# Performance work log

Measured on AMD Instinct MI355X. Metric: run time of the kernel, lower is better.

## Reference

```python
import jax, jax.numpy as jnp
import numpy as np
import math

D_MODEL = 2048
N_HEADS = 16
BATCH = 2
SEQ = 2048
ALIBI_BIAS_MAX = 8


def alibi_bias(n_heads, seq_len, alibi_bias_max=8):
    # matches torch alibi_bias(full=False): shape [1, n_heads, 1, seq_len]
    dist = jnp.arange(1 - seq_len, 1, dtype=jnp.float32).reshape(1, 1, 1, seq_len)
    m = jnp.arange(1, n_heads + 1, dtype=jnp.float32) * (alibi_bias_max / n_heads)
    slopes = 1.0 / (2.0 ** m).reshape(1, n_heads, 1, 1)
    return dist * slopes


def setup_inputs() -> dict:
    key = jax.random.key(0)
    ks = jax.random.split(key, 5)
    d = D_MODEL
    scale = 1.0 / math.sqrt(d)
    x = jax.random.normal(ks[0], (BATCH, SEQ, d), dtype=jnp.float32)
    w_qkv = jax.random.normal(ks[1], (3 * d, d), dtype=jnp.float32) * scale
    b_qkv = jnp.zeros((3 * d,), dtype=jnp.float32)
    w_out = jax.random.normal(ks[2], (d, d), dtype=jnp.float32) * scale
    b_out = jnp.zeros((d,), dtype=jnp.float32)
    attn_mask = alibi_bias(N_HEADS, SEQ, ALIBI_BIAS_MAX)
    return {"x": x, "attn_mask": attn_mask, "w_qkv": w_qkv, "b_qkv": b_qkv,
            "w_out": w_out, "b_out": b_out}


def reference(x, attn_mask, w_qkv, b_qkv, w_out, b_out):
    B, S, D = x.shape
    H = N_HEADS
    hd = D // H
    # packed QKV projection
    qkv = x @ w_qkv.T + b_qkv                      # [B,S,3D]
    qkv = qkv.reshape(B, S, 3, H, hd)
    q, k, v = qkv[:, :, 0], qkv[:, :, 1], qkv[:, :, 2]  # [B,S,H,hd]
    scores = jnp.einsum('bqhd,bkhd->bhqk', q, k) * (1.0 / math.sqrt(hd))
    scores = scores + attn_mask                    # ALiBi additive bias [1,H,1,S]
    causal = jnp.tril(jnp.ones((S, S), dtype=bool))
    scores = jnp.where(causal, scores, -jnp.inf)
    probs = jax.nn.softmax(scores, axis=-1)        # [B,H,S,S]
    ctx = jnp.einsum('bhqk,bkhd->bqhd', probs, v).reshape(B, S, D)
    return ctx @ w_out.T + b_out
```

## Files before the change

### kernel.cpp

```cpp
#include <hip/hip_runtime.h>
#include <math.h>

typedef unsigned short u16;
typedef __attribute__((ext_vector_type(8))) short short8;
typedef __attribute__((ext_vector_type(4))) float f32x4;

#define MFMA16x16x32(a, b, c) __builtin_amdgcn_mfma_f32_16x16x32_bf16((a), (b), (c), 0, 0, 0)
#define GLL16(g, s)                                                        \
  __builtin_amdgcn_global_load_lds(                                        \
      (const __attribute__((address_space(1))) void*)(g),                  \
      (__attribute__((address_space(3))) void*)(s), 16, 0, 0)

__device__ __forceinline__ u16 f32_to_bf16(float x) {
  union { float f; unsigned u; } v; v.f = x;
  unsigned r = v.u + 0x7FFFu + ((v.u >> 16) & 1u);
  return (u16)(r >> 16);
}

__device__ __forceinline__ void cvt4(const float* in, u16* out, int j) {
  float4 v = ((const float4*)in)[j];
  ushort4 o;
  o.x = f32_to_bf16(v.x);
  o.y = f32_to_bf16(v.y);
  o.z = f32_to_bf16(v.z);
  o.w = f32_to_bf16(v.w);
  ((ushort4*)out)[j] = o;
}

__global__ void cvt_all(const float* __restrict__ x, const float* __restrict__ wq,
                        const float* __restrict__ wo, u16* __restrict__ xb,
                        u16* __restrict__ wqb, u16* __restrict__ wob) {
  const int stride = gridDim.x * blockDim.x;
  const int i = blockIdx.x * blockDim.x + threadIdx.x;
  for (int j = i; j < 2097152; j += stride) cvt4(x, xb, j);
  for (int j = i; j < 3145728; j += stride) cvt4(wq, wqb, j);
  for (int j = i; j < 1048576; j += stride) cvt4(wo, wob, j);
}

template <int OUT_BF16>
__global__ __launch_bounds__(256, 3) void gemm_k32(
    const u16* __restrict__ A,
    const u16* __restrict__ B,
    const float* __restrict__ bias,
    void* __restrict__ C,
    int M, int N, int K)
{
  __shared__ u16 As[3][4096];
  __shared__ u16 Bs[3][4096];

  const int tid = threadIdx.x;
  const int w = tid >> 6, l = tid & 63;
  const int l15 = l & 15, l4 = l >> 4;
  const int wm = w >> 1, wn = w & 1;
  const long bm = (long)blockIdx.y * 128, bn = (long)blockIdx.x * 128;
  const int NT = K >> 5;

  const int h = (l & 7) ^ (l >> 3);
  const int rowoff = 2 * (l >> 3) + (h >> 2);
  const int colofs = (h & 3) * 8;
  const int c0 = (w & 1) * 4;
  const u16* sbase = (w < 2) ? (A + bm * (long)K) : (B + bn * (long)K);
  const u16* src0 = sbase + (long)(16 * (c0 + 0) + rowoff) * K + colofs;
  const u16* src1 = sbase + (long)(16 * (c0 + 1) + rowoff) * K + colofs;
  const u16* src2 = sbase + (long)(16 * (c0 + 2) + rowoff) * K + colofs;
  const u16* src3 = sbase + (long)(16 * (c0 + 3) + rowoff) * K + colofs;

#define STAGE4(tt)                                                            \
  do {                                                                        \
    const int _b = (tt) % 3;                                                  \
    const long _ko = (long)(tt) * 32;                                         \
    u16* _d = (w < 2) ? &As[_b][c0 * 512] : &Bs[_b][c0 * 512];                \
    GLL16(src0 + _ko, _d);                                                    \
    GLL16(src1 + _ko, _d + 512);                                              \
    GLL16(src2 + _ko, _d + 1024);                                             \
    GLL16(src3 + _ko, _d + 1536);                                             \
  } while (0)

  const f32x4 z4 = {0.f, 0.f, 0.f, 0.f};
  f32x4 acc[4][4];
  #pragma unroll
  for (int m = 0; m < 4; ++m)
    #pragma unroll
    for (int n = 0; n < 4; ++n) acc[m][n] = z4;

  const int inner = ((l15 & 1) * 64 + l4 * 16) ^ ((l15 >> 1) << 4);
  const int rbase = (l15 >> 1) * 128 + inner;
  const int aOfs = wm * 4096 + rbase;
  const int bOfs = wn * 4096 + rbase;

  STAGE4(0);
  STAGE4(1);
  asm volatile("s_waitcnt vmcnt(4)" ::: "memory");
  __builtin_amdgcn_s_barrier();

  for (int t = 0; t < NT; ++t) {
    const char* aT = (const char*)&As[t % 3][0];
    const char* bT = (const char*)&Bs[t % 3][0];
    short8 af[4], bf[4];
    #pragma unroll
    for (int m = 0; m < 4; ++m) af[m] = *(const short8*)(aT + aOfs + m * 1024);
    #pragma unroll
    for (int n = 0; n < 4; ++n) bf[n] = *(const short8*)(bT + bOfs + n * 1024);
    if (t + 2 < NT) {
      STAGE4(t + 2);
      asm volatile("s_waitcnt vmcnt(4) lgkmcnt(0)" ::: "memory");
    } else {
      asm volatile("s_waitcnt vmcnt(0) lgkmcnt(0)" ::: "memory");
    }
    __builtin_amdgcn_s_setprio(1);
    #pragma unroll
    for (int m = 0; m < 4; ++m)
      #pragma unroll
      for (int n = 0; n < 4; ++n)
        acc[m][n] = MFMA16x16x32(af[m], bf[n], acc[m][n]);
    __builtin_amdgcn_s_setprio(0);
    __builtin_amdgcn_s_barrier();
  }
#undef STAGE4

  #pragma unroll
  for (int m = 0; m < 4; ++m) {
    const long row0 = bm + wm * 64 + m * 16 + l4 * 4;
    #pragma unroll
    for (int n = 0; n < 4; ++n) {
      const long col = bn + wn * 64 + n * 16 + l15;
      const float bv = bias[col];
      #pragma unroll
      for (int r = 0; r < 4; ++r) {
        const float v = acc[m][n][r] + bv;
        if (OUT_BF16)
          ((u16*)C)[(row0 + r) * (long)N + col] = f32_to_bf16(v);
        else
          ((float*)C)[(row0 + r) * (long)N + col] = v;
      }
    }
  }
}

__global__ __launch_bounds__(256) void repack_kv(
    const u16* __restrict__ qkv, u16* __restrict__ kimg, u16* __restrict__ vimg)
{
  const int t = blockIdx.x;
  const int h = blockIdx.y, b = blockIdx.z;
  const int tid = threadIdx.x;
  __shared__ u16 Vl[64][136];

  const long qbase = ((long)(b * 2048 + t * 64)) * 6144 + h * 128;
  u16* kout = kimg + (((long)(b * 16 + h) * 32 + t) * 8192);
  u16* vout = vimg + (((long)(b * 16 + h) * 32 + t) * 8192);

  #pragma unroll
  for (int i = 0; i < 4; ++i) {
    const int j = tid + i * 256;
    {
      const int r = j >> 4, c8 = (j & 15) * 8;
      uint4 v = *(const uint4*)(qkv + qbase + (long)r * 6144 + 4096 + c8);
      *(uint4*)(&Vl[r][c8]) = v;
    }
    {
      const int byte = j * 16;
      const int r = byte >> 8;
      const int wv = (byte & 255) ^ ((r & 7) << 4);
      const int d0 = wv >> 1;
      uint4 v = *(const uint4*)(qkv + qbase + (long)r * 6144 + 2048 + d0);
      *(uint4*)(kout + j * 8) = v;
    }
  }
  __syncthreads();
  #pragma unroll
  for (int i = 0; i < 4; ++i) {
    const int j = tid + i * 256;
    const int byte = j * 16;
    const int d = byte >> 7;
    const int wv = (byte & 127) ^ ((d & 7) << 4);
    const int k0 = wv >> 1;
    u16 tmp[8];
    #pragma unroll
    for (int m = 0; m < 8; ++m) tmp[m] = Vl[k0 + m][d];
    *(uint4*)(vout + j * 8) = *(const uint4*)tmp;
  }
}

__global__ __launch_bounds__(256) void attn_kernel(
    const u16* __restrict__ qkv,
    const u16* __restrict__ kimg,
    const u16* __restrict__ vimg,
    u16* __restrict__ ctx)
{
  const int S = 2048, NHD = 6144, NT = 32;
  const int p = blockIdx.x, h = blockIdx.y, b = blockIdx.z;
  const int tid = threadIdx.x;
  const int w = tid >> 6, l = tid & 63;
  const int l15 = l & 15, l4 = l >> 4;

  __shared__ u16 Ks[64 * 128];
  __shared__ u16 Vt[128 * 64];
  __shared__ u16 Ps[4][16 * 64];

  const float LOG2E = 1.44269504088896f;
  const float c1 = 0.08838834764831845f * LOG2E;
  const float slope2 = exp2f(-0.5f * (float)(h + 1)) * LOG2E;

  const f32x4 z4 = {0.f, 0.f, 0.f, 0.f};

  for (int pass = 0; pass < 2; ++pass) {
    const int qblk = pass ? (NT - 1 - p) : p;
    const int qb0 = qblk * 64;

    short8 qf[4];
    {
      const int qrow = qb0 + w * 16 + l15;
      const u16* qp = qkv + (long)(b * S + qrow) * NHD + h * 128 + l4 * 8;
      #pragma unroll
      for (int kc = 0; kc < 4; ++kc) qf[kc] = *(const short8*)(qp + kc * 32);
    }

    f32x4 o[8];
    #pragma unroll
    for (int i = 0; i < 8; ++i) o[i] = z4;
    float m_r[4] = {-3.0e38f, -3.0e38f, -3.0e38f, -3.0e38f};
    float l_r[4] = {0.f, 0.f, 0.f, 0.f};

    for (int kt = 0; kt <= qblk; ++kt) {
      const u16* ksrc = kimg + (((long)(b * 16 + h) * NT + kt) * 8192);
      const u16* vsrc = vimg + (((long)(b * 16 + h) * NT + kt) * 8192);
      #pragma unroll
      for (int i = 0; i < 4; ++i) {
        const int chunk = w * 4 + i;
        __builtin_amdgcn_global_load_lds(
            (const __attribute__((address_space(1))) void*)(ksrc + chunk * 512 + l * 8),
            (__attribute__((address_space(3))) void*)(Ks + chunk * 512), 16, 0, 0);
        __builtin_amdgcn_global_load_lds(
            (const __attribute__((address_space(1))) void*)(vsrc + chunk * 512 + l * 8),
            (__attribute__((address_space(3))) void*)(Vt + chunk * 512), 16, 0, 0);
      }
      __syncthreads();

      f32x4 sf[4];
      #pragma unroll
      for (int nt = 0; nt < 4; ++nt) sf[nt] = z4;
      #pragma unroll
      for (int nt = 0; nt < 4; ++nt) {
        const int krow = nt * 16 + l15;
        #pragma unroll
        for (int kc = 0; kc < 4; ++kc) {
          int kbyte = (krow * 256 + kc * 64 + l4 * 16) ^ ((krow & 7) << 4);
          const short8 kf = *(const short8*)((const char*)Ks + kbyte);
          sf[nt] = MFMA16x16x32(qf[kc], kf, sf[nt]);
        }
      }

      float add_nt[4];
      int kg_nt[4];
      #pragma unroll
      for (int nt = 0; nt < 4; ++nt) {
        kg_nt[nt] = kt * 64 + nt * 16 + l15;
        add_nt[nt] = slope2 * (float)(kg_nt[nt] - (S - 1));
      }
      const bool diag = (kt == qblk);
      float sc[4][4], mxv[4];
      #pragma unroll
      for (int r = 0; r < 4; ++r) {
        const int qg = qb0 + w * 16 + l4 * 4 + r;
        #pragma unroll
        for (int nt = 0; nt < 4; ++nt) {
          float s = sf[nt][r] * c1 + add_nt[nt];
          if (diag && kg_nt[nt] > qg) s = -3.0e38f;
          sc[r][nt] = s;
        }
        mxv[r] = fmaxf(fmaxf(sc[r][0], sc[r][1]), fmaxf(sc[r][2], sc[r][3]));
      }
      #pragma unroll
      for (int d = 1; d < 16; d <<= 1) {
        #pragma unroll
        for (int r = 0; r < 4; ++r)
          mxv[r] = fmaxf(mxv[r], __shfl_xor(mxv[r], d, 64));
      }
      float alpha[4], sum[4];
      #pragma unroll
      for (int r = 0; r < 4; ++r) {
        const float mnew = fmaxf(m_r[r], mxv[r]);
        sum[r] = 0.f;
        #pragma unroll
        for (int nt = 0; nt < 4; ++nt) {
          const float pv = exp2f(sc[r][nt] - mnew);
          sc[r][nt] = pv;
          sum[r] += pv;
        }
        alpha[r] = exp2f(m_r[r] - mnew);
        m_r[r] = mnew;
      }
      #pragma unroll
      for (int d = 1; d < 16; d <<= 1) {
        #pragma unroll
        for (int r = 0; r < 4; ++r) sum[r] += __shfl_xor(sum[r], d, 64);
      }
      #pragma unroll
      for (int r = 0; r < 4; ++r) l_r[r] = l_r[r] * alpha[r] + sum[r];

      #pragma unroll
      for (int r = 0; r < 4; ++r) {
        const int qrow_l = l4 * 4 + r;
        #pragma unroll
        for (int nt = 0; nt < 4; ++nt) {
          int pbyte = ((qrow_l * 64 + nt * 16 + l15) * 2) ^ ((qrow_l & 7) << 4);
          *(u16*)((char*)&Ps[w][0] + pbyte) = f32_to_bf16(sc[r][nt]);
        }
      }

      #pragma unroll
      for (int nt = 0; nt < 8; ++nt)
        #pragma unroll
        for (int r = 0; r < 4; ++r) o[nt][r] *= alpha[r];

      #pragma unroll
      for (int kc = 0; kc < 2; ++kc) {
        int pbyte = ((l15 * 64 + kc * 32 + l4 * 8) * 2) ^ ((l15 & 7) << 4);
        const short8 pf = *(const short8*)((const char*)&Ps[w][0] + pbyte);
        #pragma unroll
        for (int nt = 0; nt < 8; ++nt) {
          const int d = nt * 16 + l15;
          const int vbyte = ((d * 128 + kc * 64 + l4 * 16)) ^ ((d & 7) << 4);
          const short8 vf = *(const short8*)((const char*)Vt + vbyte);
          o[nt] = MFMA16x16x32(pf, vf, o[nt]);
        }
      }
      __syncthreads();
    }

    float rl[4];
    #pragma unroll
    for (int r = 0; r < 4; ++r) rl[r] = 1.0f / l_r[r];
    #pragma unroll
    for (int nt = 0; nt < 8; ++nt) {
      #pragma unroll
      for (int r = 0; r < 4; ++r) {
        const int qg = qb0 + w * 16 + l4 * 4 + r;
        ctx[(long)(b * S + qg) * 2048 + h * 128 + nt * 16 + l15] =
            f32_to_bf16(o[nt][r] * rl[r]);
      }
    }
  }
}

extern "C" void kernel_launch(void* const* d_in, const int* in_sizes, int n_in,
                              void* d_out, int out_size, void* d_ws, size_t ws_size,
                              hipStream_t stream) {
  const float* x     = (const float*)d_in[0];
  const float* w_qkv = (const float*)d_in[2];
  const float* b_qkv = (const float*)d_in[3];
  const float* w_out = (const float*)d_in[4];
  const float* b_out = (const float*)d_in[5];
  float* out = (float*)d_out;

  char* ws = (char*)d_ws;
  u16* xb    = (u16*)(ws);
  u16* wqkvb = (u16*)(ws + 16777216UL);
  u16* woutb = (u16*)(ws + 41943040UL);
  u16* qkvb  = (u16*)(ws + 50331648UL);
  u16* ctxb  = (u16*)(ws + 100663296UL);
  u16* kimg  = (u16*)(ws);
  u16* vimg  = (u16*)(ws + 16777216UL);

  cvt_all<<<2048, 256, 0, stream>>>(x, w_qkv, w_out, xb, wqkvb, woutb);

  gemm_k32<1><<<dim3(48, 32), 256, 0, stream>>>(xb, wqkvb, b_qkv, (void*)qkvb, 4096, 6144, 2048);

  repack_kv<<<dim3(32, 16, 2), 256, 0, stream>>>(qkvb, kimg, vimg);

  attn_kernel<<<dim3(16, 16, 2), 256, 0, stream>>>(qkvb, kimg, vimg, ctxb);

  gemm_k32<0><<<dim3(16, 32), 256, 0, stream>>>(ctxb, woutb, b_out, (void*)out, 4096, 2048, 2048);
}
```

Baseline: 303.3 us.

## Add 256x256 eight-phase pipelined GEMM for QKV projection

Adds a new 512-thread GEMM kernel with 256x256 tiles and K-step 64. It splits each iteration into eight phases that interleave global-to-LDS loads, swizzled LDS fragment reads and MFMA bursts, with priority boosts around the MFMAs. Block IDs are remapped in XCD-aware order. The QKV projection now uses this kernel instead of the 128x128 gemm_k32, aiming at better data reuse and load/compute overlap. The cost is one block per 256x256 tile (384 blocks total), more registers per thread, and a large number of barriers.

```diff
diff --git a/kernel.cpp b/kernel.cpp
--- a/kernel.cpp
+++ b/kernel.cpp
@@ -38,11 +38,251 @@
 }
 
 template <int OUT_BF16>
-__global__ __launch_bounds__(256, 3) void gemm_k32(
+__global__ __launch_bounds__(512, 2) void gemm_8ph(
     const u16* __restrict__ A,
     const u16* __restrict__ B,
     const float* __restrict__ bias,
     void* __restrict__ C,
+    int M, int N, int K, int gn)
+{
+  __shared__ __attribute__((aligned(16))) u16 As[2][2][8192];
+  __shared__ __attribute__((aligned(16))) u16 Bs[2][2][8192];
+
+  const int tid = threadIdx.x;
+  const int w = tid >> 6, l = tid & 63;
+  const int l15 = l & 15, l4 = l >> 4;
+  const int wm = w >> 2, wn = w & 3;
+
+  const int cpx = gridDim.x >> 3;
+  const int sid = (blockIdx.x & 7) * cpx + (blockIdx.x >> 3);
+  const long bm = (long)(sid / gn) * 256;
+  const long bn = (long)(sid % gn) * 256;
+
+  const int NT = K >> 6, NI = NT >> 1;
+
+  const int r0 = tid >> 3;
+  const int cb0 = ((tid * 16) & 127) ^ ((r0 & 7) << 4);
+  const u16* aS = A + (bm + r0) * (long)K + (cb0 >> 1);
+  const u16* bS = B + (bn + r0) * (long)K + (cb0 >> 1);
+  const long rK64 = 64 * (long)K, rK128 = 128 * (long)K;
+  const int ldst = w * 512;
+
+#define STG(dstp, srcp, half, tt)                                            \
+  do {                                                                       \
+    GLL16((srcp) + (half) * rK128 + (long)(tt) * 64, (dstp) + ldst);         \
+    GLL16((srcp) + (half) * rK128 + rK64 + (long)(tt) * 64,                  \
+          (dstp) + ldst + 4096);                                             \
+  } while (0)
+
+  const f32x4 z4 = {0.f, 0.f, 0.f, 0.f};
+  f32x4 acc[8][4];
+  #pragma unroll
+  for (int m = 0; m < 8; ++m)
+    #pragma unroll
+    for (int n = 0; n < 4; ++n) acc[m][n] = z4;
+
+  const int swz = (l15 & 7) << 4;
+  const int xo0 = (l4 * 16) ^ swz;
+  const int xo1 = (64 + l4 * 16) ^ swz;
+  const char* aRd0 = (const char*)&As[0][wm][0] + l15 * 128;
+  const char* aRd1 = (const char*)&As[1][wm][0] + l15 * 128;
+  const char* bRd0 = (const char*)&Bs[0][wn >> 1][0] + ((wn & 1) * 64 + l15) * 128;
+  const char* bRd1 = (const char*)&Bs[1][wn >> 1][0] + ((wn & 1) * 64 + l15) * 128;
+
+  STG(&Bs[0][0][0], bS, 0, 0);
+  STG(&Bs[0][1][0], bS, 1, 0);
+  STG(&As[0][0][0], aS, 0, 0);
+  STG(&As[0][1][0], aS, 1, 0);
+  STG(&Bs[1][0][0], bS, 0, 1);
+  STG(&Bs[1][1][0], bS, 1, 1);
+  asm volatile("s_waitcnt vmcnt(4)" ::: "memory");
+  asm volatile("s_barrier" ::: "memory");
+
+  for (int j = 0; j < NI; ++j) {
+    const int t1 = 2 * j + 1;
+    const bool more = (j + 1) < NI;
+    short8 af[4][2], bf[4][2];
+
+    #pragma unroll
+    for (int m = 0; m < 4; ++m) {
+      af[m][0] = *(const short8*)(aRd0 + m * 2048 + xo0);
+      af[m][1] = *(const short8*)(aRd0 + m * 2048 + xo1);
+    }
+    #pragma unroll
+    for (int n = 0; n < 2; ++n) {
+      bf[n][0] = *(const short8*)(bRd0 + n * 2048 + xo0);
+      bf[n][1] = *(const short8*)(bRd0 + n * 2048 + xo1);
+    }
+    STG(&As[1][0][0], aS, 0, t1);
+    asm volatile("s_barrier" ::: "memory");
+    asm volatile("s_waitcnt lgkmcnt(0)" ::: "memory");
+    __builtin_amdgcn_s_setprio(1);
+    #pragma unroll
+    for (int m = 0; m < 4; ++m)
+      #pragma unroll
+      for (int n = 0; n < 2; ++n) {
+        acc[m][n] = MFMA16x16x32(af[m][0], bf[n][0], acc[m][n]);
+        acc[m][n] = MFMA16x16x32(af[m][1], bf[n][1], acc[m][n]);
+      }
+    __builtin_amdgcn_s_setprio(0);
+    asm volatile("s_barrier" ::: "memory");
+
+    #pragma unroll
+    for (int n = 2; n < 4; ++n) {
+      bf[n][0] = *(const short8*)(bRd0 + n * 2048 + xo0);
+      bf[n][1] = *(const short8*)(bRd0 + n * 2048 + xo1);
+    }
+    STG(&As[1][1][0], aS, 1, t1);
+    asm volatile("s_barrier" ::: "memory");
+    asm volatile("s_waitcnt lgkmcnt(0)" ::: "memory");
+    __builtin_amdgcn_s_setprio(1);
+    #pragma unroll
+    for (int m = 0; m < 4; ++m)
+      #pragma unroll
+      for (int n = 2; n < 4; ++n) {
+        acc[m][n] = MFMA16x16x32(af[m][0], bf[n][0], acc[m][n]);
+        acc[m][n] = MFMA16x16x32(af[m][1], bf[n][1], acc[m][n]);
+      }
+    __builtin_amdgcn_s_setprio(0);
+    asm volatile("s_barrier" ::: "memory");
+
+    #pragma unroll
+    for (int m = 0; m < 4; ++m) {
+      af[m][0] = *(const short8*)(aRd0 + 8192 + m * 2048 + xo0);
+      af[m][1] = *(const short8*)(aRd0 + 8192 + m * 2048 + xo1);
+    }
+    if (more) STG(&Bs[0][0][0], bS, 0, t1 + 1);
+    asm volatile("s_barrier" ::: "memory");
+    asm volatile("s_waitcnt lgkmcnt(0)" ::: "memory");
+    __builtin_amdgcn_s_setprio(1);
+    #pragma unroll
+    for (int m = 0; m < 4; ++m)
+      #pragma unroll
+      for (int n = 0; n < 2; ++n) {
+        acc[4 + m][n] = MFMA16x16x32(af[m][0], bf[n][0], acc[4 + m][n]);
+        acc[4 + m][n] = MFMA16x16x32(af[m][1], bf[n][1], acc[4 + m][n]);
+      }
+    __builtin_amdgcn_s_setprio(0);
+    asm volatile("s_barrier" ::: "memory");
+
+    if (more) STG(&Bs[0][1][0], bS, 1, t1 + 1);
+    asm volatile("s_barrier" ::: "memory");
+    __builtin_amdgcn_s_setprio(1);
+    #pragma unroll
+    for (int m = 0; m < 4; ++m)
+      #pragma unroll
+      for (int n = 2; n < 4; ++n) {
+        acc[4 + m][n] = MFMA16x16x32(af[m][0], bf[n][0], acc[4 + m][n]);
+        acc[4 + m][n] = MFMA16x16x32(af[m][1], bf[n][1], acc[4 + m][n]);
+      }
+    __builtin_amdgcn_s_setprio(0);
+    if (more) asm volatile("s_waitcnt vmcnt(4)" ::: "memory");
+    else      asm volatile("s_waitcnt vmcnt(0)" ::: "memory");
+    asm volatile("s_barrier" ::: "memory");
+
+    #pragma unroll
+    for (int m = 0; m < 4; ++m) {
+      af[m][0] = *(const short8*)(aRd1 + m * 2048 + xo0);
+      af[m][1] = *(const short8*)(aRd1 + m * 2048 + xo1);
+    }
+    #pragma unroll
+    for (int n = 0; n < 2; ++n) {
+      bf[n][0] = *(const short8*)(bRd1 + n * 2048 + xo0);
+      bf[n][1] = *(const short8*)(bRd1 + n * 2048 + xo1);
+    }
+    if (more) STG(&As[0][0][0], aS, 0, t1 + 1);
+    asm volatile("s_barrier" ::: "memory");
+    asm volatile("s_waitcnt lgkmcnt(0)" ::: "memory");
+    __builtin_amdgcn_s_setprio(1);
+    #pragma unroll
+    for (int m = 0; m < 4; ++m)
+      #pragma unroll
+      for (int n = 0; n < 2; ++n) {
+        acc[m][n] = MFMA16x16x32(af[m][0], bf[n][0], acc[m][n]);
+        acc[m][n] = MFMA16x16x32(af[m][1], bf[n][1], acc[m][n]);
+      }
+    __builtin_amdgcn_s_setprio(0);
+    asm volatile("s_barrier" ::: "memory");
+
+    #pragma unroll
+    for (int n = 2; n < 4; ++n) {
+      bf[n][0] = *(const short8*)(bRd1 + n * 2048 + xo0);
+      bf[n][1] = *(const short8*)(bRd1 + n * 2048 + xo1);
+    }
+    if (more) STG(&As[0][1][0], aS, 1, t1 + 1);
+    asm volatile("s_barrier" ::: "memory");
+    asm volatile("s_waitcnt lgkmcnt(0)" ::: "memory");
+    __builtin_amdgcn_s_setprio(1);
+    #pragma unroll
+    for (int m = 0; m < 4; ++m)
+      #pragma unroll
+      for (int n = 2; n < 4; ++n) {
+        acc[m][n] = MFMA16x16x32(af[m][0], bf[n][0], acc[m][n]);
+        acc[m][n] = MFMA16x16x32(af[m][1], bf[n][1], acc[m][n]);
+      }
+    __builtin_amdgcn_s_setprio(0);
+    asm volatile("s_barrier" ::: "memory");
+
+    #pragma unroll
+    for (int m = 0; m < 4; ++m) {
+      af[m][0] = *(const short8*)(aRd1 + 8192 + m * 2048 + xo0);
+      af[m][1] = *(const short8*)(aRd1 + 8192 + m * 2048 + xo1);
+    }
+    if (more) STG(&Bs[1][0][0], bS, 0, t1 + 2);
+    asm volatile("s_barrier" ::: "memory");
+    asm volatile("s_waitcnt lgkmcnt(0)" ::: "memory");
+    __builtin_amdgcn_s_setprio(1);
+    #pragma unroll
+    for (int m = 0; m < 4; ++m)
+      #pragma unroll
+      for (int n = 0; n < 2; ++n) {
+        acc[4 + m][n] = MFMA16x16x32(af[m][0], bf[n][0], acc[4 + m][n]);
+        acc[4 + m][n] = MFMA16x16x32(af[m][1], bf[n][1], acc[4 + m][n]);
+      }
+    __builtin_amdgcn_s_setprio(0);
+    asm volatile("s_barrier" ::: "memory");
+
+    if (more) STG(&Bs[1][1][0], bS, 1, t1 + 2);
+    asm volatile("s_barrier" ::: "memory");
+    __builtin_amdgcn_s_setprio(1);
+    #pragma unroll
+    for (int m = 0; m < 4; ++m)
+      #pragma unroll
+      for (int n = 2; n < 4; ++n) {
+        acc[4 + m][n] = MFMA16x16x32(af[m][0], bf[n][0], acc[4 + m][n]);
+        acc[4 + m][n] = MFMA16x16x32(af[m][1], bf[n][1], acc[4 + m][n]);
+      }
+    __builtin_amdgcn_s_setprio(0);
+    if (more) {
+      asm volatile("s_waitcnt vmcnt(4)" ::: "memory");
+      asm volatile("s_barrier" ::: "memory");
+    }
+  }
+#undef STG
+
+  #pragma unroll
+  for (int m = 0; m < 8; ++m) {
+    const long row0 = bm + wm * 128 + m * 16 + l4 * 4;
+    #pragma unroll
+    for (int n = 0; n < 4; ++n) {
+      const long col = bn + wn * 64 + n * 16 + l15;
+      const float bv = bias[col];
+      #pragma unroll
+      for (int r = 0; r < 4; ++r) {
+        const float v = acc[m][n][r] + bv;
+        if (OUT_BF16)
+          ((u16*)C)[(row0 + r) * (long)N + col] = f32_to_bf16(v);
+        else
+          ((float*)C)[(row0 + r) * (long)N + col] = v;
+      }
+    }
+  }
+}
+
+template <int OUT_BF16>
+__global__ __launch_bounds__(256, 3) void gemm_k32(
+    const u16* __restrict__ A, const u16* __restrict__ B,
+    const float* __restrict__ bias, void* __restrict__ C,
     int M, int N, int K)
 {
   __shared__ u16 As[3][4096];
@@ -364,7 +604,7 @@
 
   cvt_all<<<2048, 256, 0, stream>>>(x, w_qkv, w_out, xb, wqkvb, woutb);
 
-  gemm_k32<1><<<dim3(48, 32), 256, 0, stream>>>(xb, wqkvb, b_qkv, (void*)qkvb, 4096, 6144, 2048);
+  gemm_8ph<1><<<384, 512, 0, stream>>>(xb, wqkvb, b_qkv, (void*)qkvb, 4096, 6144, 2048, 24);
 
   repack_kv<<<dim3(32, 16, 2), 256, 0, stream>>>(qkvb, kimg, vimg);
 
```

New measurement: 306.2 us. About the same (+1.0%).
